# Kernel optimization log

Measured on AMD Instinct MI355X. Metric: run time of the kernel, lower is better.

## Reference

```python
import jax, jax.numpy as jnp
import numpy as np

N, E, G = 10000, 160000, 64          # nodes, edges, graphs
T, FIN, ED, FOUT = 5, 75, 50, 15     # towers, channels, edge-emb dim, per-tower out
EPS_BN, EPS_STD = 1e-5, 1e-5


def setup_inputs() -> dict:
    key = jax.random.key(0)
    ks = jax.random.split(key, 16)
    s = 0.05
    return dict(
        x=jax.random.randint(ks[0], (N,), 0, 21),
        edge_index=jax.random.randint(ks[1], (2, E), 0, N),
        edge_attr=jax.random.randint(ks[2], (E,), 0, 4),
        batch=jnp.sort(jax.random.randint(ks[3], (N,), 0, G)),
        node_emb=jax.random.normal(ks[4], (21, FIN), dtype=jnp.float32),
        edge_emb=jax.random.normal(ks[5], (4, ED), dtype=jnp.float32),
        We=jax.random.normal(ks[6], (4, ED, FIN), dtype=jnp.float32) * s,
        be=jnp.zeros((4, FIN), jnp.float32),
        Wpre=jax.random.normal(ks[7], (4, T, 3 * FIN, FIN), dtype=jnp.float32) * s,
        bpre=jnp.zeros((4, T, FIN), jnp.float32),
        Wpost=jax.random.normal(ks[8], (4, T, 13 * FIN, FOUT), dtype=jnp.float32) * s,
        bpost=jnp.zeros((4, T, FOUT), jnp.float32),
        Wlin=jax.random.normal(ks[9], (4, FIN, FIN), dtype=jnp.float32) * s,
        blin=jnp.zeros((4, FIN), jnp.float32),
        bn_gamma=jnp.ones((4, FIN), jnp.float32),
        bn_beta=jnp.zeros((4, FIN), jnp.float32),
        uaf=jnp.array([1.1, -0.01, 1e-5, -0.9, 1e-5], dtype=jnp.float32),
        mW1=jax.random.normal(ks[10], (FIN, 50), dtype=jnp.float32) * s,
        mb1=jnp.zeros((50,), jnp.float32),
        mW2=jax.random.normal(ks[11], (50, 25), dtype=jnp.float32) * s,
        mb2=jnp.zeros((25,), jnp.float32),
        mW3=jax.random.normal(ks[12], (25, 1), dtype=jnp.float32) * s,
        mb3=jnp.zeros((1,), jnp.float32),
    )


def _uaf(v, p):
    # softplus(A*(x+B) + C*x^2) - softplus(D*(x-B)) + E
    return (jax.nn.softplus(p[0] * (v + p[1]) + p[2] * v * v)
            - jax.nn.softplus(p[3] * (v - p[1])) + p[4])


def _pna_layer(h, src, dst, e_feat, We, be, Wpre, bpre, Wpost, bpost, Wl, bl,
               deg, avg_log):
    eemb = e_feat @ We + be                      # [E, FIN] edge encoder
    x_i, x_j = h[dst], h[src]                    # [E, FIN] gathers
    # pre-MLP: per-tower Linear(cat[x_i, x_j, e], 3F -> F), split weight blocks
    W1, W2, W3 = Wpre[:, :FIN], Wpre[:, FIN:2 * FIN], Wpre[:, 2 * FIN:]
    m = (jnp.einsum('ec,tcf->etf', x_i, W1)
         + jnp.einsum('ec,tcf->etf', x_j, W2)
         + jnp.einsum('ec,tcf->etf', eemb, W3) + bpre)   # [E, T, FIN]
    degc = jnp.maximum(deg, 1.0)[:, None, None]
    mean = jax.ops.segment_sum(m, dst, N) / degc          # [N, T, FIN]
    mean_sq = jax.ops.segment_sum(m * m, dst, N) / degc
    empty = (deg == 0.0)[:, None, None]
    mn = jnp.where(empty, 0.0, jax.ops.segment_min(m, dst, N))
    mx = jnp.where(empty, 0.0, jax.ops.segment_max(m, dst, N))
    std = jnp.sqrt(jax.nn.relu(mean_sq - mean * mean) + EPS_STD)
    agg = jnp.concatenate([mean, mn, mx, std], axis=-1)   # [N, T, 4F]
    amp = (jnp.log(jnp.maximum(deg, 1.0) + 1.0) / avg_log)[:, None, None]
    out = jnp.concatenate([agg, agg * amp, agg / amp], axis=-1)  # [N, T, 12F]
    # cat tower input (divide_input=False -> full x per tower)
    out = jnp.concatenate(
        [jnp.broadcast_to(h[:, None, :], (N, T, FIN)), out], axis=-1)  # [N,T,13F]
    out = jnp.einsum('ntc,tcf->ntf', out, Wpost) + bpost  # [N, T, FOUT]
    return out.reshape(N, T * FOUT) @ Wl + bl             # [N, FIN]


def reference(node_emb, edge_emb, We, be, Wpre, bpre, Wpost, bpost, Wlin, blin,
              bn_gamma, bn_beta, uaf, mW1, mb1, mW2, mb2, mW3, mb3,
              x, edge_index, edge_attr, batch):
    src, dst = edge_index[0], edge_index[1]
    h = node_emb[x]                              # [N, 75]
    e_feat = edge_emb[edge_attr]                 # [E, 50]
    deg = jax.ops.segment_sum(jnp.ones((E,), h.dtype), dst, N)
    avg_log = jnp.mean(jnp.log(deg + 1.0))       # PNA avg degree (log) statistic
    for l in range(4):
        out = _pna_layer(h, src, dst, e_feat, We[l], be[l], Wpre[l], bpre[l],
                         Wpost[l], bpost[l], Wlin[l], blin[l], deg, avg_log)
        mu = out.mean(axis=0)
        var = out.var(axis=0)                    # biased, training-mode BN
        out = (out - mu) * jax.lax.rsqrt(var + EPS_BN) * bn_gamma[l] + bn_beta[l]
        h = _uaf(out, uaf)
    pooled = jax.ops.segment_sum(h, batch, G)    # global_add_pool -> [G, 75]
    z = _uaf(pooled @ mW1 + mb1, uaf)
    z = _uaf(z @ mW2 + mb2, uaf)
    return z @ mW3 + mb3                         # [G, 1]
```

## Files before the change

### kernel.cpp

```cpp
#include <hip/hip_runtime.h>
#include <hip/hip_fp16.h>
#include <math.h>

static constexpr int N_   = 10000;
static constexpr int E_   = 160000;
static constexpr int G_   = 64;
static constexpr int T_   = 5;
static constexpr int FIN_ = 75;
static constexpr int ED_  = 50;
static constexpr int FOUT_= 15;
static constexpr int TF_  = T_*FIN_;
static constexpr int AGGW_= 4*FIN_;
static constexpr int YC_  = 48;
static constexpr int NP_  = 10048;
static constexpr int AW_  = 400;

__device__ __forceinline__ float softplus_f(float x){
    return fmaxf(x, 0.f) + log1pf(expf(-fabsf(x)));
}
__device__ __forceinline__ float uaf_f(float v, const float* __restrict__ p){
    return softplus_f(p[0]*(v + p[1]) + p[2]*v*v) - softplus_f(p[3]*(v - p[1])) + p[4];
}
__device__ __forceinline__ unsigned pack2h(float a, float b){
    __half2 h = __floats2half2_rn(a, b);
    return *reinterpret_cast<unsigned*>(&h);
}

__global__ void k_h0(const int* __restrict__ x, const float* __restrict__ node_emb, float* __restrict__ hT){
    int i = blockIdx.x*blockDim.x + threadIdx.x;
    if (i >= FIN_*N_) return;
    int q = i / N_, n = i % N_;
    hT[(size_t)q*NP_ + n] = node_emb[x[n]*FIN_ + q];
}

__global__ void k_deg(const int* __restrict__ ei, int* __restrict__ deg_i){
    int e = blockIdx.x*blockDim.x + threadIdx.x;
    if (e >= E_) return;
    atomicAdd(&deg_i[ei[E_ + e]], 1);
}

__global__ void k_scan(const int* __restrict__ deg_i, int* __restrict__ offs, float* __restrict__ avglog){
    __shared__ int sd[1024];
    __shared__ float sf[1024];
    __shared__ int carry;
    if (threadIdx.x == 0) carry = 0;
    __syncthreads();
    float ls = 0.f;
    for (int base = 0; base < N_; base += 1024){
        int i = base + threadIdx.x;
        int v = (i < N_) ? deg_i[i] : 0;
        if (i < N_) ls += logf((float)v + 1.f);
        sd[threadIdx.x] = v;
        __syncthreads();
        for (int off = 1; off < 1024; off <<= 1){
            int t = (threadIdx.x >= off) ? sd[threadIdx.x - off] : 0;
            __syncthreads();
            sd[threadIdx.x] += t;
            __syncthreads();
        }
        if (i < N_) offs[i] = carry + sd[threadIdx.x] - v;
        __syncthreads();
        if (threadIdx.x == 0) carry += sd[1023];
        __syncthreads();
    }
    if (threadIdx.x == 0) offs[N_] = carry;
    sf[threadIdx.x] = ls;
    __syncthreads();
    for (int off = 512; off > 0; off >>= 1){
        if (threadIdx.x < off) sf[threadIdx.x] += sf[threadIdx.x + off];
        __syncthreads();
    }
    if (threadIdx.x == 0) avglog[0] = sf[0] / (float)N_;
}

__global__ void k_fill(const int* __restrict__ ei, const int* __restrict__ eattr,
                       const int* __restrict__ offs, int* __restrict__ cursor, int* __restrict__ csr){
    int e = blockIdx.x*blockDim.x + threadIdx.x;
    if (e >= E_) return;
    int d = ei[E_ + e];
    int pos = offs[d] + atomicAdd(&cursor[d], 1);
    csr[pos] = ei[e] | (eattr[e] << 16);
}

__global__ void k_amp(const int* __restrict__ deg_i, const float* __restrict__ avglog,
                      float* __restrict__ ampv, float* __restrict__ iampv){
    int n = blockIdx.x*blockDim.x + threadIdx.x;
    if (n >= N_) return;
    float dm = fmaxf((float)deg_i[n], 1.f);
    float a = logf(dm + 1.f) / avglog[0];
    ampv[n] = a;
    iampv[n] = 1.f / a;
}

__global__ void k_eemb(const float* __restrict__ edge_emb, const float* __restrict__ We,
                       const float* __restrict__ be, float* __restrict__ eembw){
    int i = blockIdx.x*blockDim.x + threadIdx.x;
    if (i >= 4*4*FIN_) return;
    int c = i % FIN_;
    int a = (i / FIN_) % 4;
    int l = i / (4*FIN_);
    float s = be[l*FIN_ + c];
    for (int k = 0; k < ED_; k++) s = fmaf(edge_emb[a*ED_ + k], We[(l*ED_ + k)*FIN_ + c], s);
    eembw[i] = s;
}

__global__ void k_tbl(const float* __restrict__ eembw, const float* __restrict__ Wpre,
                      const float* __restrict__ bpre, float* __restrict__ tbl){
    int i = blockIdx.x*blockDim.x + threadIdx.x;
    if (i >= 4*4*TF_) return;
    int f = i % FIN_;
    int t = (i / FIN_) % T_;
    int a = (i / TF_) % 4;
    int l = i / (4*TF_);
    float s = bpre[(l*T_ + t)*FIN_ + f];
    const float* em = eembw + (l*4 + a)*FIN_;
    const float* W3 = Wpre + ((size_t)(l*T_ + t)*225 + 2*FIN_)*FIN_;
    for (int c = 0; c < FIN_; c++) s = fmaf(em[c], W3[c*FIN_ + f], s);
    tbl[i] = s;
}

__global__ void k_wcomb(const float* __restrict__ Wpost, float* __restrict__ Wcomb){
    int i = blockIdx.x*blockDim.x + threadIdx.x;
    if (i >= 4*T_*TF_*YC_) return;
    int j = i % YC_;
    int c = (i / YC_) % TF_;
    int t = (i / (YC_*TF_)) % T_;
    int l = i / (YC_*TF_*T_);
    float v = 0.f;
    if (j < 45){
        int blk = j / 15, fo = j % 15;
        const float* Wp = Wpost + (size_t)(l*T_ + t)*975*15;
        if (c < FIN_){ if (blk == 0) v = Wp[c*15 + fo]; }
        else {
            int r = c - FIN_;
            int fi = r >> 2, kind = r & 3;
            int jj = kind*FIN_ + fi;
            v = Wp[(FIN_ + blk*AGGW_ + jj)*15 + fo];
        }
    }
    Wcomb[i] = v;
}

__global__ void k_wlin80(const float* __restrict__ Wlin, float* __restrict__ Wlin80){
    int i = blockIdx.x*blockDim.x + threadIdx.x;
    if (i >= 4*FIN_*80) return;
    int q = i % 80;
    int p = (i / 80) % FIN_;
    int l = i / (80*FIN_);
    Wlin80[i] = (q < FIN_) ? Wlin[(l*FIN_ + p)*FIN_ + q] : 0.f;
}

__global__ void __launch_bounds__(256) k_A2(const float* __restrict__ hT, const float* __restrict__ Wpre_l,
                                            float* __restrict__ Af, __half* __restrict__ Bh){
    __shared__ float Act[FIN_*128];
    __shared__ float Wt[FIN_*80];
    int chunk = blockIdx.y;
    int t = chunk >> 1, half = chunk & 1;
    const float* __restrict__ W = Wpre_l + (size_t)(t*225 + half*FIN_)*FIN_;
    int n0 = blockIdx.x * 128;
    int tid = threadIdx.x;
    for (int i = tid; i < FIN_*80; i += 256){
        int r = i / 80, c = i - r*80;
        Wt[i] = (c < FIN_) ? W[r*FIN_ + c] : 0.f;
    }
    for (int i = tid; i < FIN_*128; i += 256){
        int r = i >> 7, n = i & 127;
        Act[i] = hT[(size_t)r*NP_ + n0 + n];
    }
    __syncthreads();
    int tn = tid & 31, tj = tid >> 5;
    float acc[4][10];
    #pragma unroll
    for (int m = 0; m < 4; m++)
        #pragma unroll
        for (int j = 0; j < 10; j++) acc[m][j] = 0.f;
    #pragma unroll 5
    for (int k = 0; k < FIN_; k++){
        float4 av = *(const float4*)(Act + (k<<7) + (tn<<2));
        const float* wr = Wt + k*80 + tj*10;
        #pragma unroll
        for (int j = 0; j < 10; j++){
            float wv = wr[j];
            acc[0][j] = fmaf(av.x, wv, acc[0][j]);
            acc[1][j] = fmaf(av.y, wv, acc[1][j]);
            acc[2][j] = fmaf(av.z, wv, acc[2][j]);
            acc[3][j] = fmaf(av.w, wv, acc[3][j]);
        }
    }
    int nodeb = n0 + tn*4;
    #pragma unroll
    for (int m = 0; m < 4; m++){
        int node = nodeb + m;
        if (node >= N_) continue;
        if (half == 0){
            float2* dst = (float2*)(Af + (size_t)node*AW_ + t*80 + tj*10);
            #pragma unroll
            for (int j = 0; j < 5; j++) dst[j] = make_float2(acc[m][2*j], acc[m][2*j+1]);
        } else {
            unsigned* dst = (unsigned*)(Bh + (size_t)node*AW_ + t*80 + tj*10);
            #pragma unroll
            for (int j = 0; j < 5; j++) dst[j] = pack2h(acc[m][2*j], acc[m][2*j+1]);
        }
    }
}

__global__ void __launch_bounds__(128) k_agg(const float* __restrict__ Af, const __half* __restrict__ Bh,
                                             const int* __restrict__ offs, const int* __restrict__ csr,
                                             const float* __restrict__ tbl_l, float4* __restrict__ agg2){
    __shared__ float tl[4*TF_];
    int bid = blockIdx.x;
    int n = (bid & 7)*1250 + (bid >> 3);
    for (int idx = threadIdx.x; idx < 4*TF_; idx += 128) tl[idx] = tbl_l[idx];
    __syncthreads();
    int s = offs[n], e_end = offs[n+1];
    int f0 = threadIdx.x;
    int f1 = threadIdx.x + 128;
    int f2r = threadIdx.x + 256;
    int f2 = (f2r < TF_) ? f2r : 0;
    int ao0 = (f0/FIN_)*80 + f0%FIN_;
    int ao1 = (f1/FIN_)*80 + f1%FIN_;
    int ao2 = (f2/FIN_)*80 + f2%FIN_;
    const float* An = Af + (size_t)n*AW_;
    float a0 = An[ao0], a1 = An[ao1], a2 = An[ao2];
    float s0=0.f,s1=0.f,s2=0.f, q0=0.f,q1=0.f,q2=0.f;
    float mn0=INFINITY,mn1=INFINITY,mn2=INFINITY;
    float mx0=-INFINITY,mx1=-INFINITY,mx2=-INFINITY;
    for (int e = s; e < e_end; e++){
        int pk = csr[e];
        int src = pk & 0xFFFF;
        int at = pk >> 16;
        const __half* B = Bh + (size_t)src*AW_;
        const float* tt = tl + at*TF_;
        float m0 = a0 + __half2float(B[ao0]) + tt[f0];
        float m1 = a1 + __half2float(B[ao1]) + tt[f1];
        float m2 = a2 + __half2float(B[ao2]) + tt[f2];
        s0 += m0; s1 += m1; s2 += m2;
        q0 = fmaf(m0,m0,q0); q1 = fmaf(m1,m1,q1); q2 = fmaf(m2,m2,q2);
        mn0 = fminf(mn0,m0); mn1 = fminf(mn1,m1); mn2 = fminf(mn2,m2);
        mx0 = fmaxf(mx0,m0); mx1 = fmaxf(mx1,m1); mx2 = fmaxf(mx2,m2);
    }
    float deg = (float)(e_end - s);
    float dc = fmaxf(deg, 1.f);
    float inv = 1.f / dc;
    bool empty = (deg == 0.f);
    {
        float mean = s0*inv;
        float sd = sqrtf(fmaxf(q0*inv - mean*mean, 0.f) + 1e-5f);
        int t = f0/FIN_, fi = f0%FIN_;
        agg2[(size_t)(t*FIN_+fi)*NP_ + n] = make_float4(mean, empty?0.f:mn0, empty?0.f:mx0, sd);
    }
    {
        float mean = s1*inv;
        float sd = sqrtf(fmaxf(q1*inv - mean*mean, 0.f) + 1e-5f);
        int t = f1/FIN_, fi = f1%FIN_;
        agg2[(size_t)(t*FIN_+fi)*NP_ + n] = make_float4(mean, empty?0.f:mn1, empty?0.f:mx1, sd);
    }
    if (f2r < TF_){
        float mean = s2*inv;
        float sd = sqrtf(fmaxf(q2*inv - mean*mean, 0.f) + 1e-5f);
        int t = f2r/FIN_, fi = f2r%FIN_;
        agg2[(size_t)(t*FIN_+fi)*NP_ + n] = make_float4(mean, empty?0.f:mn2, empty?0.f:mx2, sd);
    }
}

__global__ void __launch_bounds__(256) k_post4(const float* __restrict__ hT, const float4* __restrict__ agg2,
                                               const float* __restrict__ Wcomb_l, float* __restrict__ YbT){
    __shared__ float Act[25*128];
    __shared__ float Wt[25*YC_];
    int t = blockIdx.y;
    int n0 = blockIdx.x * 128;
    int tid = threadIdx.x;
    int tn = tid & 31, tj = tid >> 5;
    const float* __restrict__ W = Wcomb_l + (size_t)t*TF_*YC_;
    float acc[4][6];
    #pragma unroll
    for (int m = 0; m < 4; m++)
        #pragma unroll
        for (int j = 0; j < 6; j++) acc[m][j] = 0.f;

    for (int ch = 0; ch < 3; ch++){
        __syncthreads();
        for (int i = tid; i < 25*YC_; i += 256) Wt[i] = W[ch*25*YC_ + i];
        for (int i = tid; i < 25*128; i += 256){
            int r = i >> 7, n = i & 127;
            Act[i] = hT[(size_t)(ch*25 + r)*NP_ + n0 + n];
        }
        __syncthreads();
        #pragma unroll
        for (int k = 0; k < 25; k++){
            float4 av = *(const float4*)(Act + (k<<7) + (tn<<2));
            const float* wr = Wt + k*YC_ + tj*6;
            #pragma unroll
            for (int j = 0; j < 6; j++){
                float wv = wr[j];
                acc[0][j] = fmaf(av.x, wv, acc[0][j]);
                acc[1][j] = fmaf(av.y, wv, acc[1][j]);
                acc[2][j] = fmaf(av.z, wv, acc[2][j]);
                acc[3][j] = fmaf(av.w, wv, acc[3][j]);
            }
        }
    }
    const float4* ag = agg2 + (size_t)t*FIN_*NP_;
    for (int ch = 0; ch < 15; ch++){
        __syncthreads();
        for (int i = tid; i < 20*YC_; i += 256) Wt[i] = W[(FIN_ + ch*20)*YC_ + i];
        for (int i = tid; i < 5*128; i += 256){
            int fq = i >> 7, n = i & 127;
            float4 v = ag[(size_t)(ch*5 + fq)*NP_ + n0 + n];
            Act[(fq*4+0)*128 + n] = v.x;
            Act[(fq*4+1)*128 + n] = v.y;
            Act[(fq*4+2)*128 + n] = v.z;
            Act[(fq*4+3)*128 + n] = v.w;
        }
        __syncthreads();
        #pragma unroll
        for (int k = 0; k < 20; k++){
            float4 av = *(const float4*)(Act + (k<<7) + (tn<<2));
            const float* wr = Wt + k*YC_ + tj*6;
            #pragma unroll
            for (int j = 0; j < 6; j++){
                float wv = wr[j];
                acc[0][j] = fmaf(av.x, wv, acc[0][j]);
                acc[1][j] = fmaf(av.y, wv, acc[1][j]);
                acc[2][j] = fmaf(av.z, wv, acc[2][j]);
                acc[3][j] = fmaf(av.w, wv, acc[3][j]);
            }
        }
    }
    int nodeb = n0 + tn*4;
    #pragma unroll
    for (int j = 0; j < 6; j++){
        int col = t*YC_ + tj*6 + j;
        float4 v = make_float4(acc[0][j], acc[1][j], acc[2][j], acc[3][j]);
        if (nodeb + 3 < N_){
            *(float4*)(YbT + (size_t)col*NP_ + nodeb) = v;
        } else {
            #pragma unroll
            for (int m = 0; m < 4; m++)
                if (nodeb + m < N_) YbT[(size_t)col*NP_ + nodeb + m] = (&v.x)[m];
        }
    }
}

__global__ void __launch_bounds__(64) k_Y(const float* __restrict__ YbT, const float* __restrict__ ampv,
                                          const float* __restrict__ iampv, const float* __restrict__ bpost_l,
                                          const float* __restrict__ Wlin80_l, const float* __restrict__ blin_l,
                                          float* __restrict__ olinT, float* __restrict__ bnsum, float* __restrict__ bnsq){
    __shared__ float st[64*77];
    int qbase = blockIdx.y * 40;
    int qcnt  = blockIdx.y ? 35 : 40;
    int n = blockIdx.x*64 + threadIdx.x;
    int nn = (n < N_) ? n : N_-1;
    bool valid = (n < N_);
    float amp = ampv[nn], iamp = iampv[nn];
    #pragma unroll 1
    for (int t = 0; t < T_; t++){
        #pragma unroll
        for (int fo = 0; fo < FOUT_; fo++){
            float v = YbT[(size_t)(t*YC_ + fo)*NP_ + nn]
                    + amp  * YbT[(size_t)(t*YC_ + 15 + fo)*NP_ + nn]
                    + iamp * YbT[(size_t)(t*YC_ + 30 + fo)*NP_ + nn]
                    + bpost_l[t*FOUT_ + fo];
            st[threadIdx.x*77 + t*FOUT_ + fo] = v;
        }
    }
    __syncthreads();
    float acc[40];
    #pragma unroll
    for (int k = 0; k < 40; k++) acc[k] = (qbase + k < FIN_) ? blin_l[qbase + k] : 0.f;
    #pragma unroll 1
    for (int p = 0; p < FIN_; p++){
        float yv = st[threadIdx.x*77 + p];
        const float* Wp = Wlin80_l + p*80 + qbase;
        #pragma unroll
        for (int k = 0; k < 40; k++) acc[k] = fmaf(yv, Wp[k], acc[k]);
    }
    if (valid){
        #pragma unroll
        for (int k = 0; k < 40; k++){
            int q = qbase + k;
            if (q < FIN_) olinT[(size_t)q*NP_ + n] = acc[k];
        }
    }
    __syncthreads();
    #pragma unroll
    for (int k = 0; k < 40; k++) st[threadIdx.x*77 + k] = valid ? acc[k] : 0.f;
    __syncthreads();
    for (int qq = threadIdx.x; qq < qcnt; qq += 64){
        float s = 0.f, s2 = 0.f;
        #pragma unroll 4
        for (int m = 0; m < 64; m++){ float v = st[m*77 + qq]; s += v; s2 = fmaf(v, v, s2); }
        atomicAdd(&bnsum[qbase + qq], s);
        atomicAdd(&bnsq[qbase + qq], s2);
    }
}

__global__ void k_bn(const float* __restrict__ olinT, const float* __restrict__ bnsum, const float* __restrict__ bnsq,
                     const float* __restrict__ gamma_l, const float* __restrict__ beta_l,
                     const float* __restrict__ uafp, float* __restrict__ hT){
    int i = blockIdx.x*blockDim.x + threadIdx.x;
    if (i >= FIN_*N_) return;
    int q = i / N_, n = i % N_;
    float mu = bnsum[q] * (1.f/(float)N_);
    float var = bnsq[q] * (1.f/(float)N_) - mu*mu;
    float xh = (olinT[(size_t)q*NP_ + n] - mu) * rsqrtf(var + 1e-5f) * gamma_l[q] + beta_l[q];
    hT[(size_t)q*NP_ + n] = uaf_f(xh, uafp);
}

__global__ void __launch_bounds__(256) k_pool2(const float* __restrict__ hT, const int* __restrict__ batch,
                                               float* __restrict__ pooled){
    __shared__ int sb[2];
    int g = blockIdx.x;
    if (threadIdx.x < 2){
        int key = g + threadIdx.x;
        int lo = 0, hi = N_;
        while (lo < hi){ int mid = (lo + hi) >> 1; if (batch[mid] < key) lo = mid + 1; else hi = mid; }
        sb[threadIdx.x] = lo;
    }
    __syncthreads();
    int s = sb[0], e = sb[1];
    int wave = threadIdx.x >> 6, lane = threadIdx.x & 63;
    for (int q = wave; q < FIN_; q += 4){
        float sum = 0.f;
        for (int n = s + lane; n < e; n += 64) sum += hT[(size_t)q*NP_ + n];
        #pragma unroll
        for (int off = 32; off > 0; off >>= 1) sum += __shfl_down(sum, off);
        if (lane == 0) pooled[g*FIN_ + q] = sum;
    }
}

__global__ void __launch_bounds__(64) k_mlp(const float* __restrict__ pooled,
        const float* __restrict__ mW1, const float* __restrict__ mb1,
        const float* __restrict__ mW2, const float* __restrict__ mb2,
        const float* __restrict__ mW3, const float* __restrict__ mb3,
        const float* __restrict__ uafp, float* __restrict__ outp){
    __shared__ float pr[FIN_];
    __shared__ float z1[50];
    __shared__ float z2[25];
    int g = blockIdx.x;
    for (int c = threadIdx.x; c < FIN_; c += 64) pr[c] = pooled[g*FIN_ + c];
    __syncthreads();
    if (threadIdx.x < 50){
        float s = mb1[threadIdx.x];
        for (int c = 0; c < FIN_; c++) s = fmaf(pr[c], mW1[c*50 + threadIdx.x], s);
        z1[threadIdx.x] = uaf_f(s, uafp);
    }
    __syncthreads();
    if (threadIdx.x < 25){
        float s = mb2[threadIdx.x];
        for (int c = 0; c < 50; c++) s = fmaf(z1[c], mW2[c*25 + threadIdx.x], s);
        z2[threadIdx.x] = uaf_f(s, uafp);
    }
    __syncthreads();
    if (threadIdx.x == 0){
        float s = mb3[0];
        for (int c = 0; c < 25; c++) s = fmaf(z2[c], mW3[c], s);
        outp[g] = s;
    }
}

extern "C" void kernel_launch(void* const* d_in, const int* in_sizes, int n_in,
                              void* d_out, int out_size, void* d_ws, size_t ws_size,
                              hipStream_t stream) {
    const int* x         = (const int*)d_in[0];
    const int* ei        = (const int*)d_in[1];
    const int* eattr     = (const int*)d_in[2];
    const int* batch     = (const int*)d_in[3];
    const float* node_emb= (const float*)d_in[4];
    const float* edge_emb= (const float*)d_in[5];
    const float* We      = (const float*)d_in[6];
    const float* be      = (const float*)d_in[7];
    const float* Wpre    = (const float*)d_in[8];
    const float* bpre    = (const float*)d_in[9];
    const float* Wpost   = (const float*)d_in[10];
    const float* bpost   = (const float*)d_in[11];
    const float* Wlin    = (const float*)d_in[12];
    const float* blin    = (const float*)d_in[13];
    const float* bn_gamma= (const float*)d_in[14];
    const float* bn_beta = (const float*)d_in[15];
    const float* uafp    = (const float*)d_in[16];
    const float* mW1     = (const float*)d_in[17];
    const float* mb1     = (const float*)d_in[18];
    const float* mW2     = (const float*)d_in[19];
    const float* mb2     = (const float*)d_in[20];
    const float* mW3     = (const float*)d_in[21];
    const float* mb3     = (const float*)d_in[22];
    float* outp          = (float*)d_out;

    char* w = (char*)d_ws;
    auto alloc = [&](size_t bytes) -> void* {
        void* p = (void*)w;
        w += (bytes + 255) & ~(size_t)255;
        return p;
    };
    float*  hT    = (float*)alloc((size_t)FIN_*NP_*4);
    float*  Af    = (float*)alloc((size_t)N_*AW_*4);
    __half* Bh    = (__half*)alloc((size_t)N_*AW_*2);
    float4* agg2  = (float4*)alloc((size_t)TF_*NP_*16);
    float*  YbT   = Af;
    float*  olinT = Af + 3000000;
    float*  ampv  = (float*)alloc(N_*4);
    float*  iampv = (float*)alloc(N_*4);
    float*  avglog= (float*)alloc(4);
    float*  tbl   = (float*)alloc(4*4*TF_*4);
    float*  eembw = (float*)alloc(4*4*FIN_*4);
    float*  Wcomb = (float*)alloc((size_t)4*T_*TF_*YC_*4);
    float*  Wlin80= (float*)alloc(4*FIN_*80*4);
    float*  bnsum = (float*)alloc(2*FIN_*4);
    float*  bnsq  = bnsum + FIN_;
    float*  pooled= (float*)alloc(G_*FIN_*4);
    int* deg_i   = (int*)alloc(N_*4);
    int* offs    = (int*)alloc((N_+1)*4);
    int* cursor  = (int*)alloc(N_*4);
    int* csr     = (int*)alloc(E_*4);

    hipMemsetAsync(deg_i, 0, N_*4, stream);
    hipMemsetAsync(cursor, 0, N_*4, stream);

    k_h0<<<(FIN_*N_ + 255)/256, 256, 0, stream>>>(x, node_emb, hT);
    k_deg<<<(E_ + 255)/256, 256, 0, stream>>>(ei, deg_i);
    k_scan<<<1, 1024, 0, stream>>>(deg_i, offs, avglog);
    k_fill<<<(E_ + 255)/256, 256, 0, stream>>>(ei, eattr, offs, cursor, csr);
    k_amp<<<(N_ + 255)/256, 256, 0, stream>>>(deg_i, avglog, ampv, iampv);
    k_eemb<<<(4*4*FIN_ + 255)/256, 256, 0, stream>>>(edge_emb, We, be, eembw);
    k_tbl<<<(4*4*TF_ + 255)/256, 256, 0, stream>>>(eembw, Wpre, bpre, tbl);
    k_wcomb<<<(4*T_*TF_*YC_ + 255)/256, 256, 0, stream>>>(Wpost, Wcomb);
    k_wlin80<<<(4*FIN_*80 + 255)/256, 256, 0, stream>>>(Wlin, Wlin80);

    int nmb = (N_ + 127)/128;
    int nrb = (N_ + 63)/64;
    for (int l = 0; l < 4; l++){
        hipMemsetAsync(bnsum, 0, 2*FIN_*4, stream);
        k_A2<<<dim3(nmb, 10), 256, 0, stream>>>(hT, Wpre + (size_t)l*T_*225*FIN_, Af, Bh);
        k_agg<<<N_, 128, 0, stream>>>(Af, Bh, offs, csr, tbl + (size_t)l*4*TF_, agg2);
        k_post4<<<dim3(nmb, T_), 256, 0, stream>>>(hT, agg2, Wcomb + (size_t)l*T_*TF_*YC_, YbT);
        k_Y<<<dim3(nrb, 2), 64, 0, stream>>>(YbT, ampv, iampv, bpost + l*T_*FOUT_,
                                             Wlin80 + (size_t)l*FIN_*80, blin + l*FIN_,
                                             olinT, bnsum, bnsq);
        k_bn<<<(FIN_*N_ + 255)/256, 256, 0, stream>>>(olinT, bnsum, bnsq,
                                                      bn_gamma + l*FIN_, bn_beta + l*FIN_, uafp, hT);
    }

    k_pool2<<<G_, 256, 0, stream>>>(hT, batch, pooled);
    k_mlp<<<G_, 64, 0, stream>>>(pooled, mW1, mb1, mW2, mb2, mW3, mb3, uafp, outp);
}
```

Measured before the change: 1.017 ms.

## Store aggregates as planar arrays and double-buffer the post-GEMM tile loads

The aggregation kernel now writes mean/min/max/std as four separate planar rows per tower channel instead of interleaved float4 records. The post-MLP GEMM can then load activation tiles with coalesced float4 copies instead of transposing them through shared memory. The post kernel is rewritten as one uniform 19-chunk K loop over padded hT (80 rows) and the aggregate planes. It prefetches the next chunk into registers and double-buffers the shared tiles, leaving one barrier per chunk. To support this, node padding grows to 10112, hT gains five zero rows, and the combined weight matrix is re-laid out with zero rows, which adds a little padded work and memory.

```diff
diff --git a/kernel.cpp b/kernel.cpp
--- a/kernel.cpp
+++ b/kernel.cpp
@@ -12,8 +12,9 @@
 static constexpr int TF_  = T_*FIN_;
 static constexpr int AGGW_= 4*FIN_;
 static constexpr int YC_  = 48;
-static constexpr int NP_  = 10048;
+static constexpr int NP_  = 10112;
 static constexpr int AW_  = 400;
+static constexpr int WK_  = 380;
 
 __device__ __forceinline__ float softplus_f(float x){
     return fmaxf(x, 0.f) + log1pf(expf(-fabsf(x)));
@@ -28,9 +29,9 @@
 
 __global__ void k_h0(const int* __restrict__ x, const float* __restrict__ node_emb, float* __restrict__ hT){
     int i = blockIdx.x*blockDim.x + threadIdx.x;
-    if (i >= FIN_*N_) return;
+    if (i >= 80*N_) return;
     int q = i / N_, n = i % N_;
-    hT[(size_t)q*NP_ + n] = node_emb[x[n]*FIN_ + q];
+    hT[(size_t)q*NP_ + n] = (q < FIN_) ? node_emb[x[n]*FIN_ + q] : 0.f;
 }
 
 __global__ void k_deg(const int* __restrict__ ei, int* __restrict__ deg_i){
@@ -121,21 +122,19 @@
 
 __global__ void k_wcomb(const float* __restrict__ Wpost, float* __restrict__ Wcomb){
     int i = blockIdx.x*blockDim.x + threadIdx.x;
-    if (i >= 4*T_*TF_*YC_) return;
+    if (i >= 4*T_*WK_*YC_) return;
     int j = i % YC_;
-    int c = (i / YC_) % TF_;
-    int t = (i / (YC_*TF_)) % T_;
-    int l = i / (YC_*TF_*T_);
+    int c = (i / YC_) % WK_;
+    int t = (i / (YC_*WK_)) % T_;
+    int l = i / (YC_*WK_*T_);
     float v = 0.f;
     if (j < 45){
         int blk = j / 15, fo = j % 15;
         const float* Wp = Wpost + (size_t)(l*T_ + t)*975*15;
         if (c < FIN_){ if (blk == 0) v = Wp[c*15 + fo]; }
-        else {
-            int r = c - FIN_;
-            int fi = r >> 2, kind = r & 3;
-            int jj = kind*FIN_ + fi;
-            v = Wp[(FIN_ + blk*AGGW_ + jj)*15 + fo];
+        else if (c >= 80){
+            int r = c - 80;
+            v = Wp[(FIN_ + blk*AGGW_ + r)*15 + fo];
         }
     }
     Wcomb[i] = v;
@@ -206,7 +205,7 @@
 
 __global__ void __launch_bounds__(128) k_agg(const float* __restrict__ Af, const __half* __restrict__ Bh,
                                              const int* __restrict__ offs, const int* __restrict__ csr,
-                                             const float* __restrict__ tbl_l, float4* __restrict__ agg2){
+                                             const float* __restrict__ tbl_l, float* __restrict__ aggT){
     __shared__ float tl[4*TF_];
     int bid = blockIdx.x;
     int n = (bid & 7)*1250 + (bid >> 3);
@@ -243,53 +242,79 @@
     float dc = fmaxf(deg, 1.f);
     float inv = 1.f / dc;
     bool empty = (deg == 0.f);
+    const size_t K75 = (size_t)FIN_*NP_;
     {
         float mean = s0*inv;
         float sd = sqrtf(fmaxf(q0*inv - mean*mean, 0.f) + 1e-5f);
         int t = f0/FIN_, fi = f0%FIN_;
-        agg2[(size_t)(t*FIN_+fi)*NP_ + n] = make_float4(mean, empty?0.f:mn0, empty?0.f:mx0, sd);
+        float* o = aggT + ((size_t)(t*AGGW_ + fi))*NP_ + n;
+        o[0] = mean; o[K75] = empty?0.f:mn0; o[2*K75] = empty?0.f:mx0; o[3*K75] = sd;
     }
     {
         float mean = s1*inv;
         float sd = sqrtf(fmaxf(q1*inv - mean*mean, 0.f) + 1e-5f);
         int t = f1/FIN_, fi = f1%FIN_;
-        agg2[(size_t)(t*FIN_+fi)*NP_ + n] = make_float4(mean, empty?0.f:mn1, empty?0.f:mx1, sd);
+        float* o = aggT + ((size_t)(t*AGGW_ + fi))*NP_ + n;
+        o[0] = mean; o[K75] = empty?0.f:mn1; o[2*K75] = empty?0.f:mx1; o[3*K75] = sd;
     }
     if (f2r < TF_){
         float mean = s2*inv;
         float sd = sqrtf(fmaxf(q2*inv - mean*mean, 0.f) + 1e-5f);
         int t = f2r/FIN_, fi = f2r%FIN_;
-        agg2[(size_t)(t*FIN_+fi)*NP_ + n] = make_float4(mean, empty?0.f:mn2, empty?0.f:mx2, sd);
-    }
-}
-
-__global__ void __launch_bounds__(256) k_post4(const float* __restrict__ hT, const float4* __restrict__ agg2,
+        float* o = aggT + ((size_t)(t*AGGW_ + fi))*NP_ + n;
+        o[0] = mean; o[K75] = empty?0.f:mn2; o[2*K75] = empty?0.f:mx2; o[3*K75] = sd;
+    }
+}
+
+__global__ void __launch_bounds__(256) k_post5(const float* __restrict__ hT, const float* __restrict__ aggT,
                                                const float* __restrict__ Wcomb_l, float* __restrict__ YbT){
-    __shared__ float Act[25*128];
-    __shared__ float Wt[25*YC_];
+    __shared__ float Act[2][20*128];
+    __shared__ float Wt[2][20*YC_];
     int t = blockIdx.y;
     int n0 = blockIdx.x * 128;
     int tid = threadIdx.x;
     int tn = tid & 31, tj = tid >> 5;
-    const float* __restrict__ W = Wcomb_l + (size_t)t*TF_*YC_;
+    const float* __restrict__ Wl = Wcomb_l + (size_t)t*WK_*YC_;
+    const float* __restrict__ aggt = aggT + (size_t)t*AGGW_*NP_;
+
+    {
+        const float* s = hT + n0;
+        for (int i = tid; i < 640; i += 256){
+            int r = i >> 5, c4 = i & 31;
+            *(float4*)(&Act[0][r*128 + c4*4]) = *(const float4*)(s + (size_t)r*NP_ + c4*4);
+        }
+        if (tid < 240){
+            int r = tid / 12, c4 = tid % 12;
+            *(float4*)(&Wt[0][r*YC_ + c4*4]) = *(const float4*)(Wl + r*YC_ + c4*4);
+        }
+    }
+    __syncthreads();
+
     float acc[4][6];
     #pragma unroll
     for (int m = 0; m < 4; m++)
         #pragma unroll
         for (int j = 0; j < 6; j++) acc[m][j] = 0.f;
 
-    for (int ch = 0; ch < 3; ch++){
-        __syncthreads();
-        for (int i = tid; i < 25*YC_; i += 256) Wt[i] = W[ch*25*YC_ + i];
-        for (int i = tid; i < 25*128; i += 256){
-            int r = i >> 7, n = i & 127;
-            Act[i] = hT[(size_t)(ch*25 + r)*NP_ + n0 + n];
-        }
-        __syncthreads();
-        #pragma unroll
-        for (int k = 0; k < 25; k++){
-            float4 av = *(const float4*)(Act + (k<<7) + (tn<<2));
-            const float* wr = Wt + k*YC_ + tj*6;
+    #pragma unroll 1
+    for (int ch = 0; ch < 19; ch++){
+        int buf = ch & 1;
+        float4 pa0, pa1, pa2, pw;
+        if (ch + 1 < 19){
+            int ch1 = ch + 1;
+            const float* s = (ch1 < 4) ? (hT + (size_t)(ch1*20)*NP_ + n0)
+                                       : (aggt + (size_t)((ch1-4)*20)*NP_ + n0);
+            { int i0 = tid;       pa0 = *(const float4*)(s + (size_t)(i0 >> 5)*NP_ + (i0 & 31)*4); }
+            { int i1 = tid + 256; pa1 = *(const float4*)(s + (size_t)(i1 >> 5)*NP_ + (i1 & 31)*4); }
+            if (tid < 128){ int i2 = tid + 512; pa2 = *(const float4*)(s + (size_t)(i2 >> 5)*NP_ + (i2 & 31)*4); }
+            if (tid < 240){ int r = tid / 12, c4 = tid % 12; pw = *(const float4*)(Wl + (size_t)(ch1*20 + r)*YC_ + c4*4); }
+        }
+        const float* A = Act[buf];
+        const float* Wb = Wt[buf];
+        #pragma unroll
+        for (int k = 0; k < 20; k++){
+            float4 av = *(const float4*)(A + (k<<7) + (tn<<2));
+            const float* wr = Wb + k*YC_ + tj*6;
             #pragma unroll
             for (int j = 0; j < 6; j++){
                 float wv = wr[j];
@@ -299,32 +324,14 @@
                 acc[3][j] = fmaf(av.w, wv, acc[3][j]);
             }
         }
-    }
-    const float4* ag = agg2 + (size_t)t*FIN_*NP_;
-    for (int ch = 0; ch < 15; ch++){
-        __syncthreads();
-        for (int i = tid; i < 20*YC_; i += 256) Wt[i] = W[(FIN_ + ch*20)*YC_ + i];
-        for (int i = tid; i < 5*128; i += 256){
-            int fq = i >> 7, n = i & 127;
-            float4 v = ag[(size_t)(ch*5 + fq)*NP_ + n0 + n];
-            Act[(fq*4+0)*128 + n] = v.x;
-            Act[(fq*4+1)*128 + n] = v.y;
-            Act[(fq*4+2)*128 + n] = v.z;
-            Act[(fq*4+3)*128 + n] = v.w;
-        }
-        __syncthreads();
-        #pragma unroll
-        for (int k = 0; k < 20; k++){
-            float4 av = *(const float4*)(Act + (k<<7) + (tn<<2));
-            const float* wr = Wt + k*YC_ + tj*6;
-            #pragma unroll
-            for (int j = 0; j < 6; j++){
-                float wv = wr[j];
-                acc[0][j] = fmaf(av.x, wv, acc[0][j]);
-                acc[1][j] = fmaf(av.y, wv, acc[1][j]);
-                acc[2][j] = fmaf(av.z, wv, acc[2][j]);
-                acc[3][j] = fmaf(av.w, wv, acc[3][j]);
-            }
+        if (ch + 1 < 19){
+            float* Ad = Act[buf ^ 1];
+            float* Wd = Wt[buf ^ 1];
+            { int i0 = tid;       *(float4*)(&Ad[(i0 >> 5)*128 + (i0 & 31)*4]) = pa0; }
+            { int i1 = tid + 256; *(float4*)(&Ad[(i1 >> 5)*128 + (i1 & 31)*4]) = pa1; }
+            if (tid < 128){ int i2 = tid + 512; *(float4*)(&Ad[(i2 >> 5)*128 + (i2 & 31)*4]) = pa2; }
+            if (tid < 240){ int r = tid / 12, c4 = tid % 12; *(float4*)(&Wd[r*YC_ + c4*4]) = pw; }
+            __syncthreads();
         }
     }
     int nodeb = n0 + tn*4;
@@ -493,10 +500,10 @@
         w += (bytes + 255) & ~(size_t)255;
         return p;
     };
-    float*  hT    = (float*)alloc((size_t)FIN_*NP_*4);
+    float*  hT    = (float*)alloc((size_t)80*NP_*4);
     float*  Af    = (float*)alloc((size_t)N_*AW_*4);
     __half* Bh    = (__half*)alloc((size_t)N_*AW_*2);
-    float4* agg2  = (float4*)alloc((size_t)TF_*NP_*16);
+    float*  aggT  = (float*)alloc((size_t)T_*AGGW_*NP_*4);
     float*  YbT   = Af;
     float*  olinT = Af + 3000000;
     float*  ampv  = (float*)alloc(N_*4);
@@ -504,7 +511,7 @@
     float*  avglog= (float*)alloc(4);
     float*  tbl   = (float*)alloc(4*4*TF_*4);
     float*  eembw = (float*)alloc(4*4*FIN_*4);
-    float*  Wcomb = (float*)alloc((size_t)4*T_*TF_*YC_*4);
+    float*  Wcomb = (float*)alloc((size_t)4*T_*WK_*YC_*4);
     float*  Wlin80= (float*)alloc(4*FIN_*80*4);
     float*  bnsum = (float*)alloc(2*FIN_*4);
     float*  bnsq  = bnsum + FIN_;
@@ -517,14 +524,14 @@
     hipMemsetAsync(deg_i, 0, N_*4, stream);
     hipMemsetAsync(cursor, 0, N_*4, stream);
 
-    k_h0<<<(FIN_*N_ + 255)/256, 256, 0, stream>>>(x, node_emb, hT);
+    k_h0<<<(80*N_ + 255)/256, 256, 0, stream>>>(x, node_emb, hT);
     k_deg<<<(E_ + 255)/256, 256, 0, stream>>>(ei, deg_i);
     k_scan<<<1, 1024, 0, stream>>>(deg_i, offs, avglog);
     k_fill<<<(E_ + 255)/256, 256, 0, stream>>>(ei, eattr, offs, cursor, csr);
     k_amp<<<(N_ + 255)/256, 256, 0, stream>>>(deg_i, avglog, ampv, iampv);
     k_eemb<<<(4*4*FIN_ + 255)/256, 256, 0, stream>>>(edge_emb, We, be, eembw);
     k_tbl<<<(4*4*TF_ + 255)/256, 256, 0, stream>>>(eembw, Wpre, bpre, tbl);
-    k_wcomb<<<(4*T_*TF_*YC_ + 255)/256, 256, 0, stream>>>(Wpost, Wcomb);
+    k_wcomb<<<(4*T_*WK_*YC_ + 255)/256, 256, 0, stream>>>(Wpost, Wcomb);
     k_wlin80<<<(4*FIN_*80 + 255)/256, 256, 0, stream>>>(Wlin, Wlin80);
 
     int nmb = (N_ + 127)/128;
@@ -532,8 +539,8 @@
     for (int l = 0; l < 4; l++){
         hipMemsetAsync(bnsum, 0, 2*FIN_*4, stream);
         k_A2<<<dim3(nmb, 10), 256, 0, stream>>>(hT, Wpre + (size_t)l*T_*225*FIN_, Af, Bh);
-        k_agg<<<N_, 128, 0, stream>>>(Af, Bh, offs, csr, tbl + (size_t)l*4*TF_, agg2);
-        k_post4<<<dim3(nmb, T_), 256, 0, stream>>>(hT, agg2, Wcomb + (size_t)l*T_*TF_*YC_, YbT);
+        k_agg<<<N_, 128, 0, stream>>>(Af, Bh, offs, csr, tbl + (size_t)l*4*TF_, aggT);
+        k_post5<<<dim3(nmb, T_), 256, 0, stream>>>(hT, aggT, Wcomb + (size_t)l*T_*WK_*YC_, YbT);
         k_Y<<<dim3(nrb, 2), 64, 0, stream>>>(YbT, ampv, iampv, bpost + l*T_*FOUT_,
                                              Wlin80 + (size_t)l*FIN_*80, blin + l*FIN_,
                                              olinT, bnsum, bnsq);
```

After: 1.187 ms. +16.7%, slower.
